# Performance work log

Measured on AMD Instinct MI355X. Metric: run time of the kernel, lower is better.

Reference implementation:

```python
import jax, jax.numpy as jnp
import numpy as np

WS = 7        # window size
NH = 8        # num heads


def setup_inputs() -> dict:
    key = jax.random.key(0)
    ks = jax.random.split(key, 5)
    B, N, C = 32, 3136, 512
    x = jax.random.normal(ks[0], (B, N, C), dtype=jnp.float32)
    s = 1.0 / np.sqrt(C)
    w_qkv = jax.random.normal(ks[1], (C, 3 * C), dtype=jnp.float32) * s
    b_qkv = jax.random.normal(ks[2], (3 * C,), dtype=jnp.float32) * 0.01
    w_proj = jax.random.normal(ks[3], (C, C), dtype=jnp.float32) * s
    b_proj = jax.random.normal(ks[4], (C,), dtype=jnp.float32) * 0.01
    return {"x": x, "w_qkv": w_qkv, "b_qkv": b_qkv, "w_proj": w_proj, "b_proj": b_proj}


def reference(x, w_qkv, b_qkv, w_proj, b_proj):
    B, N, C = x.shape
    H = W = int(round(N ** 0.5))
    hd = C // NH
    t = WS * WS  # 49 tokens per window
    # window partition: (B,N,C) -> (nW, 49, C)
    xw = x.reshape(B, H // WS, WS, W // WS, WS, C)
    xw = jnp.transpose(xw, (0, 1, 3, 2, 4, 5)).reshape(-1, t, C)
    # qkv projection; NOTE: no head permute (faithful to source), so
    # q,k,v : (nW, 49, NH, hd)
    qkv = (xw @ w_qkv + b_qkv).reshape(-1, t, 3, NH, hd)
    q, k, v = qkv[:, :, 0], qkv[:, :, 1], qkv[:, :, 2]
    # q @ k^T contracts head_dim, attends over heads axis: (nW, 49, NH, NH)
    attn = jnp.einsum('wthd,wtgd->wthg', q, k) * (hd ** -0.5)
    attn = jax.nn.softmax(attn, axis=-1)
    out = jnp.einsum('wthg,wtgd->wthd', attn, v)          # (nW, 49, NH, hd)
    # faithful transpose(1,2).reshape(-1, 49, C) (scrambles layout, as in torch)
    out = jnp.transpose(out, (0, 2, 1, 3)).reshape(-1, t, C)
    out = out @ w_proj + b_proj
    # window merge back to (B, N, C)
    out = out.reshape(B, H // WS, W // WS, WS, WS, C)
    out = jnp.transpose(out, (0, 1, 3, 2, 4, 5)).reshape(B, N, C)
    return out
```

## Files before the change

### kernel.cpp

```cpp
#include <hip/hip_runtime.h>
#include <stdint.h>
#include <stddef.h>

typedef short s16;
typedef __attribute__((ext_vector_type(8))) short short8;
typedef __attribute__((ext_vector_type(4))) float floatx4;

__device__ __forceinline__ float bf2f(short s) {
    union { float f; uint32_t u; } c; c.u = ((uint32_t)(uint16_t)s) << 16; return c.f;
}
__device__ __forceinline__ short f2bf(float f) {
    union { float f; uint32_t u; } c; c.f = f;
    uint32_t u = c.u;
    u += 0x7fffu + ((u >> 16) & 1u);
    return (short)(u >> 16);
}

__global__ __launch_bounds__(256) void cvt_kernel(const float* __restrict__ src,
                                                  s16* __restrict__ dst) {
    size_t i = (size_t)blockIdx.x * 256 + threadIdx.x;
    const floatx4* s4 = (const floatx4*)src;
    floatx4 a = s4[i * 2], b = s4[i * 2 + 1];
    short8 o;
    o[0] = f2bf(a[0]); o[1] = f2bf(a[1]); o[2] = f2bf(a[2]); o[3] = f2bf(a[3]);
    o[4] = f2bf(b[0]); o[5] = f2bf(b[1]); o[6] = f2bf(b[2]); o[7] = f2bf(b[3]);
    ((short8*)dst)[i] = o;
}

__global__ __launch_bounds__(256) void transpose_kernel(const float* __restrict__ w,
                                                        s16* __restrict__ wt,
                                                        int K, int N) {
    int idx = blockIdx.x * 256 + threadIdx.x;
    if (idx >= K * N) return;
    int n = idx / K, k = idx - n * K;
    wt[idx] = f2bf(w[(size_t)k * N + n]);
}

__device__ __forceinline__ const s16* x_row_ptr(const s16* xb, int m) {
    int win = m / 49, t = m - win * 49;
    int b = win >> 6, rem = win & 63, hb = rem >> 3, wb = rem & 7;
    int r = t / 7, c = t - r * 7;
    int n = (hb * 7 + r) * 56 + wb * 7 + c;
    return xb + ((size_t)b * 3136 + n) * 512;
}

template <int MODE>
__global__ __launch_bounds__(512, 2) void gemm_kernel(const s16* __restrict__ A,
                                                      const s16* __restrict__ Bt,
                                                      const float* __restrict__ bias,
                                                      void* __restrict__ outp) {
    constexpr int NT  = (MODE == 0) ? 12 : 4;
    constexpr int CPX = (MODE == 0) ? 588 : 196;

    const int o  = (blockIdx.x & 7) * CPX + (blockIdx.x >> 3);
    const int tm = o / NT, tn = o - tm * NT;

    const int tid = threadIdx.x, wave = tid >> 6, lane = tid & 63;

    __shared__ s16 lA[3][256 * 64];
    __shared__ s16 lB[3][128 * 64];

    const int sub  = lane >> 3;
    const int col8 = (((lane & 7) ^ sub) << 3);
    const s16* a_src[4];
    const s16* b_src[2];
#pragma unroll
    for (int i = 0; i < 4; ++i) {
        int row = (wave * 4 + i) * 8 + sub;
        if (MODE == 0) a_src[i] = x_row_ptr(A, tm * 256 + row) + col8;
        else           a_src[i] = A + (size_t)(tm * 256 + row) * 512 + col8;
    }
#pragma unroll
    for (int i = 0; i < 2; ++i) {
        int row = (wave * 2 + i) * 8 + sub;
        b_src[i] = Bt + (size_t)(tn * 128 + row) * 512 + col8;
    }

#define STAGE(buf)                                                              \
    do {                                                                        \
        _Pragma("unroll")                                                       \
        for (int i_ = 0; i_ < 4; ++i_) {                                        \
            __builtin_amdgcn_global_load_lds(                                   \
                (const __attribute__((address_space(1))) void*)a_src[i_],       \
                (__attribute__((address_space(3))) void*)&lA[buf][(wave * 4 + i_) * 512], \
                16, 0, 0);                                                      \
            a_src[i_] += 64;                                                    \
        }                                                                       \
        _Pragma("unroll")                                                       \
        for (int i_ = 0; i_ < 2; ++i_) {                                        \
            __builtin_amdgcn_global_load_lds(                                   \
                (const __attribute__((address_space(1))) void*)b_src[i_],       \
                (__attribute__((address_space(3))) void*)&lB[buf][(wave * 2 + i_) * 512], \
                16, 0, 0);                                                      \
            b_src[i_] += 64;                                                    \
        }                                                                       \
    } while (0)

    floatx4 acc[4][4];
#pragma unroll
    for (int mt = 0; mt < 4; ++mt)
#pragma unroll
        for (int nt = 0; nt < 4; ++nt)
            acc[mt][nt] = (floatx4){0.f, 0.f, 0.f, 0.f};

    const int wm = wave >> 1, wn = wave & 1;
    const int lm = lane & 15, quad = lane >> 4;

    STAGE(0);
    STAGE(1);
    asm volatile("s_waitcnt vmcnt(6)" ::: "memory");
    __builtin_amdgcn_s_barrier();
    __builtin_amdgcn_sched_barrier(0);

#pragma unroll
    for (int kt = 0; kt < 8; ++kt) {
        if (kt + 2 < 8) STAGE((kt + 2) % 3);
        const int cur = kt % 3;

        short8 af[4][2], bq[4][2];
#pragma unroll
        for (int kk = 0; kk < 2; ++kk) {
            const int sw = (((kk << 2) | quad) ^ (lm & 7)) << 3;
#pragma unroll
            for (int mt = 0; mt < 4; ++mt)
                af[mt][kk] = *(const short8*)&lA[cur][(wm * 64 + mt * 16 + lm) * 64 + sw];
#pragma unroll
            for (int nt = 0; nt < 4; ++nt)
                bq[nt][kk] = *(const short8*)&lB[cur][(wn * 64 + nt * 16 + lm) * 64 + sw];
        }

        __builtin_amdgcn_s_setprio(1);
#pragma unroll
        for (int kk = 0; kk < 2; ++kk)
#pragma unroll
            for (int mt = 0; mt < 4; ++mt)
#pragma unroll
                for (int nt = 0; nt < 4; ++nt)
                    acc[mt][nt] = __builtin_amdgcn_mfma_f32_16x16x32_bf16(
                        af[mt][kk], bq[nt][kk], acc[mt][nt], 0, 0, 0);
        __builtin_amdgcn_s_setprio(0);

        if (kt < 7) {
            if (kt < 6) asm volatile("s_waitcnt vmcnt(6)" ::: "memory");
            else        asm volatile("s_waitcnt vmcnt(0)" ::: "memory");
            __builtin_amdgcn_s_barrier();
            __builtin_amdgcn_sched_barrier(0);
        }
    }
#undef STAGE

    float bv[4];
#pragma unroll
    for (int nt = 0; nt < 4; ++nt)
        bv[nt] = bias[tn * 128 + wn * 64 + nt * 16 + lm];

#pragma unroll
    for (int mt = 0; mt < 4; ++mt) {
        int mbase = tm * 256 + wm * 64 + mt * 16 + quad * 4;
#pragma unroll
        for (int i = 0; i < 4; ++i) {
            int m = mbase + i;
            size_t rowoff;
            if (MODE == 1) {
                int win = m / 49, t = m - win * 49;
                int b = win >> 6, rem = win & 63, hb = rem >> 3, wb = rem & 7;
                int r = t / 7, c = t - r * 7;
                int n = (hb * 7 + r) * 56 + wb * 7 + c;
                rowoff = ((size_t)b * 3136 + n) * 512;
            } else {
                rowoff = (size_t)m * 1536;
            }
#pragma unroll
            for (int nt = 0; nt < 4; ++nt) {
                int coln = tn * 128 + wn * 64 + nt * 16 + lm;
                float v = acc[mt][nt][i] + bv[nt];
                if (MODE == 0) ((s16*)outp)[rowoff + coln] = f2bf(v);
                else           ((float*)outp)[rowoff + coln] = v;
            }
        }
    }
}

__global__ __launch_bounds__(256) void attn_kernel(const s16* __restrict__ qkv,
                                                   s16* __restrict__ attn) {
    const int tid = threadIdx.x, wave = tid >> 6, lane = tid & 63;
    const int m = blockIdx.x * 4 + wave;

    __shared__ s16 sh[4][1536];
    s16* my = sh[wave];
    const s16* row = qkv + (size_t)m * 1536;
#pragma unroll
    for (int i = 0; i < 3; ++i)
        *(short8*)&my[i * 512 + lane * 8] = *(const short8*)&row[i * 512 + lane * 8];
    __syncthreads();

    const int h = lane >> 3, g = lane & 7;
    const s16* qs = my + h * 64;
    const s16* ks = my + 512 + g * 64;
    const s16* vs = my + 1024;

    float s = 0.f;
#pragma unroll
    for (int db = 0; db < 8; ++db) {
        int d0 = ((db + h) & 7) * 8;
        short8 q8 = *(const short8*)&qs[d0];
        short8 k8 = *(const short8*)&ks[d0];
#pragma unroll
        for (int j = 0; j < 8; ++j) s += bf2f(q8[j]) * bf2f(k8[j]);
    }
    s *= 0.125f;

    float mx = s;
    mx = fmaxf(mx, __shfl_xor(mx, 1));
    mx = fmaxf(mx, __shfl_xor(mx, 2));
    mx = fmaxf(mx, __shfl_xor(mx, 4));
    float p = __expf(s - mx);
    float sum = p;
    sum += __shfl_xor(sum, 1);
    sum += __shfl_xor(sum, 2);
    sum += __shfl_xor(sum, 4);
    p /= sum;

    float o[8];
#pragma unroll
    for (int j = 0; j < 8; ++j) o[j] = 0.f;
    const int dgrp = (lane & 7) * 8;
#pragma unroll
    for (int gg = 0; gg < 8; ++gg) {
        float pg = __shfl(p, h * 8 + gg);
        short8 v8 = *(const short8*)&vs[gg * 64 + dgrp];
#pragma unroll
        for (int j = 0; j < 8; ++j) o[j] += pg * bf2f(v8[j]);
    }

    int win = m / 49, t = m - win * 49;
    s16* dst = attn + (size_t)win * 25088 + h * 3136 + t * 64 + dgrp;
    short8 ob;
#pragma unroll
    for (int j = 0; j < 8; ++j) ob[j] = f2bf(o[j]);
    *(short8*)dst = ob;
}

extern "C" void kernel_launch(void* const* d_in, const int* in_sizes, int n_in,
                              void* d_out, int out_size, void* d_ws, size_t ws_size,
                              hipStream_t stream) {
    const float* x      = (const float*)d_in[0];
    const float* w_qkv  = (const float*)d_in[1];
    const float* b_qkv  = (const float*)d_in[2];
    const float* w_proj = (const float*)d_in[3];
    const float* b_proj = (const float*)d_in[4];

    char* ws = (char*)d_ws;
    s16* xbf    = (s16*)ws;
    s16* qkv    = (s16*)(ws + 102760448ull);
    s16* attn   = (s16*)(ws + 102760448ull + 308281344ull);
    s16* wqkvT  = (s16*)(ws + 102760448ull + 308281344ull + 102760448ull);
    s16* wprojT = (s16*)(ws + 102760448ull + 308281344ull + 102760448ull + 1572864ull);

    cvt_kernel<<<25088, 256, 0, stream>>>(x, xbf);
    transpose_kernel<<<3072, 256, 0, stream>>>(w_qkv, wqkvT, 512, 1536);
    transpose_kernel<<<1024, 256, 0, stream>>>(w_proj, wprojT, 512, 512);
    gemm_kernel<0><<<392 * 12, 512, 0, stream>>>(xbf, wqkvT, b_qkv, qkv);
    attn_kernel<<<25088, 256, 0, stream>>>(qkv, attn);
    gemm_kernel<1><<<392 * 4, 512, 0, stream>>>(attn, wprojT, b_proj, d_out);
}
```

Measured before the change: 833.2 us.

## Use 256x256 GEMM tiles with BK=32 and interleaved per-phase prefetch

The GEMM block tile grows from 256x128 to 256x256 and the K step shrinks from 64 to 32, so each wave now holds 8x4 MFMA accumulators and the block count halves. The LDS swizzle is dropped. The inner loop is split into four phases, each issuing one slice of the next stage's global-to-LDS loads between MFMA groups with barriers in between. The aim is more operand reuse per LDS byte and finer overlap of loads with compute. The costs are more accumulator registers, which may hurt occupancy at launch_bounds(512,2), and possible LDS bank conflicts without the swizzle.

```diff
diff --git a/kernel.cpp b/kernel.cpp
--- a/kernel.cpp
+++ b/kernel.cpp
@@ -49,114 +49,120 @@
                                                       const s16* __restrict__ Bt,
                                                       const float* __restrict__ bias,
                                                       void* __restrict__ outp) {
-    constexpr int NT  = (MODE == 0) ? 12 : 4;
-    constexpr int CPX = (MODE == 0) ? 588 : 196;
+    constexpr int NT  = (MODE == 0) ? 6 : 2;
+    constexpr int CPX = (MODE == 0) ? 294 : 98;
 
     const int o  = (blockIdx.x & 7) * CPX + (blockIdx.x >> 3);
     const int tm = o / NT, tn = o - tm * NT;
 
     const int tid = threadIdx.x, wave = tid >> 6, lane = tid & 63;
 
-    __shared__ s16 lA[3][256 * 64];
-    __shared__ s16 lB[3][128 * 64];
-
-    const int sub  = lane >> 3;
-    const int col8 = (((lane & 7) ^ sub) << 3);
-    const s16* a_src[4];
+    __shared__ s16 lA[3][256 * 32];
+    __shared__ s16 lB[3][256 * 32];
+
+    const int rloc = wave * 16 + (lane >> 2);
+    const int gran = (lane & 3) * 8;
+    const s16* a_src[2];
     const s16* b_src[2];
 #pragma unroll
-    for (int i = 0; i < 4; ++i) {
-        int row = (wave * 4 + i) * 8 + sub;
-        if (MODE == 0) a_src[i] = x_row_ptr(A, tm * 256 + row) + col8;
-        else           a_src[i] = A + (size_t)(tm * 256 + row) * 512 + col8;
-    }
-#pragma unroll
     for (int i = 0; i < 2; ++i) {
-        int row = (wave * 2 + i) * 8 + sub;
-        b_src[i] = Bt + (size_t)(tn * 128 + row) * 512 + col8;
-    }
-
-#define STAGE(buf)                                                              \
+        int row = i * 128 + rloc;
+        if (MODE == 0) a_src[i] = x_row_ptr(A, tm * 256 + row) + gran;
+        else           a_src[i] = A + (size_t)(tm * 256 + row) * 512 + gran;
+        b_src[i] = Bt + (size_t)(tn * 256 + row) * 512 + gran;
+    }
+
+#define STAGE_A(buf, i)                                                         \
     do {                                                                        \
-        _Pragma("unroll")                                                       \
-        for (int i_ = 0; i_ < 4; ++i_) {                                        \
-            __builtin_amdgcn_global_load_lds(                                   \
-                (const __attribute__((address_space(1))) void*)a_src[i_],       \
-                (__attribute__((address_space(3))) void*)&lA[buf][(wave * 4 + i_) * 512], \
-                16, 0, 0);                                                      \
-            a_src[i_] += 64;                                                    \
-        }                                                                       \
-        _Pragma("unroll")                                                       \
-        for (int i_ = 0; i_ < 2; ++i_) {                                        \
-            __builtin_amdgcn_global_load_lds(                                   \
-                (const __attribute__((address_space(1))) void*)b_src[i_],       \
-                (__attribute__((address_space(3))) void*)&lB[buf][(wave * 2 + i_) * 512], \
-                16, 0, 0);                                                      \
-            b_src[i_] += 64;                                                    \
-        }                                                                       \
+        __builtin_amdgcn_global_load_lds(                                       \
+            (const __attribute__((address_space(1))) void*)a_src[i],            \
+            (__attribute__((address_space(3))) void*)&lA[buf][(i) * 4096 + wave * 512], \
+            16, 0, 0);                                                          \
+        a_src[i] += 32;                                                         \
     } while (0)
-
-    floatx4 acc[4][4];
-#pragma unroll
-    for (int mt = 0; mt < 4; ++mt)
+#define STAGE_B(buf, i)                                                         \
+    do {                                                                        \
+        __builtin_amdgcn_global_load_lds(                                       \
+            (const __attribute__((address_space(1))) void*)b_src[i],            \
+            (__attribute__((address_space(3))) void*)&lB[buf][(i) * 4096 + wave * 512], \
+            16, 0, 0);                                                          \
+        b_src[i] += 32;                                                         \
+    } while (0)
+
+    floatx4 acc[8][4];
+#pragma unroll
+    for (int mt = 0; mt < 8; ++mt)
 #pragma unroll
         for (int nt = 0; nt < 4; ++nt)
             acc[mt][nt] = (floatx4){0.f, 0.f, 0.f, 0.f};
 
-    const int wm = wave >> 1, wn = wave & 1;
+    const int wm = wave & 1, wn = wave >> 1;
     const int lm = lane & 15, quad = lane >> 4;
-
-    STAGE(0);
-    STAGE(1);
-    asm volatile("s_waitcnt vmcnt(6)" ::: "memory");
+    const int koff = quad * 8;
+
+    STAGE_A(0, 0); STAGE_A(0, 1); STAGE_B(0, 0); STAGE_B(0, 1);
+    STAGE_A(1, 0); STAGE_A(1, 1); STAGE_B(1, 0); STAGE_B(1, 1);
+    asm volatile("s_waitcnt vmcnt(4)" ::: "memory");
     __builtin_amdgcn_s_barrier();
     __builtin_amdgcn_sched_barrier(0);
 
 #pragma unroll
-    for (int kt = 0; kt < 8; ++kt) {
-        if (kt + 2 < 8) STAGE((kt + 2) % 3);
-        const int cur = kt % 3;
-
-        short8 af[4][2], bq[4][2];
-#pragma unroll
-        for (int kk = 0; kk < 2; ++kk) {
-            const int sw = (((kk << 2) | quad) ^ (lm & 7)) << 3;
-#pragma unroll
-            for (int mt = 0; mt < 4; ++mt)
-                af[mt][kk] = *(const short8*)&lA[cur][(wm * 64 + mt * 16 + lm) * 64 + sw];
+    for (int kt = 0; kt < 16; ++kt) {
+        const int cur = kt % 3, nxt = (kt + 2) % 3;
+        short8 bq[4];
+#pragma unroll
+        for (int p = 0; p < 4; ++p) {
+            if (p == 0) {
+#pragma unroll
+                for (int nt = 0; nt < 4; ++nt)
+                    bq[nt] = *(const short8*)&lB[cur][(wn * 64 + nt * 16 + lm) * 32 + koff];
+            }
+            short8 a0 = *(const short8*)&lA[cur][(wm * 128 + (2 * p) * 16 + lm) * 32 + koff];
+            short8 a1 = *(const short8*)&lA[cur][(wm * 128 + (2 * p + 1) * 16 + lm) * 32 + koff];
+
+            if (kt < 14) {
+                if      (p == 0) STAGE_A(nxt, 0);
+                else if (p == 1) STAGE_A(nxt, 1);
+                else if (p == 2) STAGE_B(nxt, 0);
+                else             STAGE_B(nxt, 1);
+            }
+
+            __builtin_amdgcn_s_barrier();
+            asm volatile("s_waitcnt lgkmcnt(0)" ::: "memory");
+            __builtin_amdgcn_sched_barrier(0);
+
+            __builtin_amdgcn_s_setprio(1);
 #pragma unroll
             for (int nt = 0; nt < 4; ++nt)
-                bq[nt][kk] = *(const short8*)&lB[cur][(wn * 64 + nt * 16 + lm) * 64 + sw];
+                acc[2 * p][nt] = __builtin_amdgcn_mfma_f32_16x16x32_bf16(
+                    a0, bq[nt], acc[2 * p][nt], 0, 0, 0);
+#pragma unroll
+            for (int nt = 0; nt < 4; ++nt)
+                acc[2 * p + 1][nt] = __builtin_amdgcn_mfma_f32_16x16x32_bf16(
+                    a1, bq[nt], acc[2 * p + 1][nt], 0, 0, 0);
+            __builtin_amdgcn_s_setprio(0);
+
+            if (p == 3) {
+                if (kt < 14)       asm volatile("s_waitcnt vmcnt(4)" ::: "memory");
+                else if (kt == 14) asm volatile("s_waitcnt vmcnt(0)" ::: "memory");
+            }
+            if (!(kt == 15 && p == 3)) {
+                __builtin_amdgcn_s_barrier();
+                __builtin_amdgcn_sched_barrier(0);
+            }
         }
-
-        __builtin_amdgcn_s_setprio(1);
-#pragma unroll
-        for (int kk = 0; kk < 2; ++kk)
-#pragma unroll
-            for (int mt = 0; mt < 4; ++mt)
-#pragma unroll
-                for (int nt = 0; nt < 4; ++nt)
-                    acc[mt][nt] = __builtin_amdgcn_mfma_f32_16x16x32_bf16(
-                        af[mt][kk], bq[nt][kk], acc[mt][nt], 0, 0, 0);
-        __builtin_amdgcn_s_setprio(0);
-
-        if (kt < 7) {
-            if (kt < 6) asm volatile("s_waitcnt vmcnt(6)" ::: "memory");
-            else        asm volatile("s_waitcnt vmcnt(0)" ::: "memory");
-            __builtin_amdgcn_s_barrier();
-            __builtin_amdgcn_sched_barrier(0);
-        }
-    }
-#undef STAGE
+    }
+#undef STAGE_A
+#undef STAGE_B
 
     float bv[4];
 #pragma unroll
     for (int nt = 0; nt < 4; ++nt)
-        bv[nt] = bias[tn * 128 + wn * 64 + nt * 16 + lm];
-
-#pragma unroll
-    for (int mt = 0; mt < 4; ++mt) {
-        int mbase = tm * 256 + wm * 64 + mt * 16 + quad * 4;
+        bv[nt] = bias[tn * 256 + wn * 64 + nt * 16 + lm];
+
+#pragma unroll
+    for (int mt = 0; mt < 8; ++mt) {
+        int mbase = tm * 256 + wm * 128 + mt * 16 + quad * 4;
 #pragma unroll
         for (int i = 0; i < 4; ++i) {
             int m = mbase + i;
@@ -172,7 +178,7 @@
             }
 #pragma unroll
             for (int nt = 0; nt < 4; ++nt) {
-                int coln = tn * 128 + wn * 64 + nt * 16 + lm;
+                int coln = tn * 256 + wn * 64 + nt * 16 + lm;
                 float v = acc[mt][nt][i] + bv[nt];
                 if (MODE == 0) ((s16*)outp)[rowoff + coln] = f2bf(v);
                 else           ((float*)outp)[rowoff + coln] = v;
@@ -260,7 +266,7 @@
     cvt_kernel<<<25088, 256, 0, stream>>>(x, xbf);
     transpose_kernel<<<3072, 256, 0, stream>>>(w_qkv, wqkvT, 512, 1536);
     transpose_kernel<<<1024, 256, 0, stream>>>(w_proj, wprojT, 512, 512);
-    gemm_kernel<0><<<392 * 12, 512, 0, stream>>>(xbf, wqkvT, b_qkv, qkv);
+    gemm_kernel<0><<<392 * 6, 512, 0, stream>>>(xbf, wqkvT, b_qkv, qkv);
     attn_kernel<<<25088, 256, 0, stream>>>(qkv, attn);
-    gemm_kernel<1><<<392 * 4, 512, 0, stream>>>(attn, wprojT, b_proj, d_out);
-}
+    gemm_kernel<1><<<392 * 2, 512, 0, stream>>>(attn, wprojT, b_proj, d_out);
+}
```

Result: faster. 759.9 us (-8.8%).
